# Optimization experiments

Hardware: AMD Instinct MI355X
Metric: run time of the kernel (lower is better)

## Reference

```python
import jax, jax.numpy as jnp
import numpy as np

N, E, F, H, L, G, EMB, C = 50000, 600000, 128, 128, 4, 64, 64, 10
BN_EPS = 1e-5


def setup_inputs() -> dict:
    key = jax.random.key(0)
    k = lambda i: jax.random.fold_in(key, i)
    s = 0.05  # weight scale
    return {
        "x": jax.random.normal(k(0), (N, F), jnp.float32),
        "edge_index": jax.random.randint(k(1), (2, E), 0, N, jnp.int64),
        "batch": jnp.sort(jax.random.randint(k(2), (N,), 0, G, jnp.int64)),
        "emb": jax.random.normal(k(3), (G, EMB), jnp.float32),
        "eps": jnp.zeros((L,), jnp.float32),
        "W1": jax.random.normal(k(4), (L, F, H), jnp.float32) * s,
        "b1": jnp.zeros((L, H), jnp.float32),
        "W2": jax.random.normal(k(5), (L, H, H), jnp.float32) * s,
        "b2": jnp.zeros((L, H), jnp.float32),
        "gamma": jnp.ones((L, H), jnp.float32),
        "beta": jnp.zeros((L, H), jnp.float32),
        "lin1_w": jax.random.normal(k(6), (L * H + EMB, 2 * H), jnp.float32) * s,
        "lin1_b": jnp.zeros((2 * H,), jnp.float32),
        "lin2_w": jax.random.normal(k(7), (2 * H, H), jnp.float32) * s,
        "lin2_b": jnp.zeros((H,), jnp.float32),
        "lin4_w": jax.random.normal(k(8), (H, C), jnp.float32) * s,
        "lin4_b": jnp.zeros((C,), jnp.float32),
    }


def _gin_mlp(h, W1, b1, W2, b2, gamma, beta):
    # Linear -> ReLU -> Linear -> ReLU -> BatchNorm1d (batch stats)
    h = jax.nn.relu(h @ W1 + b1)
    h = jax.nn.relu(h @ W2 + b2)
    mean = jnp.mean(h, axis=0)
    var = jnp.var(h, axis=0)
    return (h - mean) * jax.lax.rsqrt(var + BN_EPS) * gamma + beta


def reference(x, edge_index, batch, emb, eps, W1, b1, W2, b2, gamma, beta,
              lin1_w, lin1_b, lin2_w, lin2_b, lin4_w, lin4_b):
    src, dst = edge_index[0], edge_index[1]
    xs = []
    for l in range(L):
        # GIN: MLP((1+eps)*x_i + sum_{j->i} x_j)  via gather + scatter-add
        agg = jax.ops.segment_sum(x[src], dst, num_segments=N)  # [N,H]
        x = _gin_mlp((1.0 + eps[l]) * x + agg,
                     W1[l], b1[l], W2[l], b2[l], gamma[l], beta[l])
        xs.append(x)
    h = jnp.concatenate(xs, axis=1)  # [N, L*H]
    # global mean pool per graph
    sums = jax.ops.segment_sum(h, batch, num_segments=G)  # [G, L*H]
    cnt = jax.ops.segment_sum(jnp.ones((N,), h.dtype), batch, num_segments=G)
    pooled = sums / jnp.maximum(cnt, 1.0)[:, None]
    z = jnp.concatenate([pooled, emb.reshape(G, -1)], axis=1)
    z = jax.nn.relu(z @ lin1_w + lin1_b)  # .relu() twice is idempotent
    # dropout p=0.5 skipped (eval mode); lin3 unused in original forward
    z = jax.nn.relu(z @ lin2_w + lin2_b)
    z = z @ lin4_w + lin4_b
    return jax.nn.log_softmax(z, axis=1)
```

## Files before the change

### kernel.cpp

```cpp
#include <hip/hip_runtime.h>
#include <cstdint>
#include <cstddef>

#define N_NODES 50000
#define N_EDGES 600000
#define NLAYER  4
#define NGRAPH  64
#define SCAN_NB 196
#define NBLK_MLP ((N_NODES + 127) / 128)

typedef unsigned int   u32;
typedef unsigned short u16;
typedef unsigned char  u8;
typedef float f32x4  __attribute__((ext_vector_type(4)));
typedef short bf16x8 __attribute__((ext_vector_type(8)));

__device__ __forceinline__ u16 f2bf(float f) {
    u32 x = __float_as_uint(f);
    u32 r = x + 0x7fffu + ((x >> 16) & 1u);
    return (u16)(r >> 16);
}
__device__ __forceinline__ u32 pack2(float a, float b) {
    return (u32)f2bf(a) | ((u32)f2bf(b) << 16);
}

__device__ __forceinline__ float fp8b0(u32 u) { return __builtin_amdgcn_cvt_f32_fp8(u, 0); }
__device__ __forceinline__ float fp8b1(u32 u) { return __builtin_amdgcn_cvt_f32_fp8(u, 1); }
__device__ __forceinline__ u32 pk_fp8(float a, float b) {
    return (u32)__builtin_amdgcn_cvt_pk_fp8_f32(a, b, 0, false);
}

__global__ __launch_bounds__(256) void cvt_x(const float4* __restrict__ x,
                                             u32* __restrict__ xf8) {
    int i = blockIdx.x * 256 + threadIdx.x;
    if (i < N_NODES * 32) {
        float4 v = x[i];
        u32 r = pk_fp8(v.x, v.y);
        r = (u32)__builtin_amdgcn_cvt_pk_fp8_f32(v.z, v.w, (int)r, true);
        xf8[i] = r;
    }
}

__global__ __launch_bounds__(128) void cvt_w(const float* __restrict__ W1,
                                             const float* __restrict__ W2,
                                             short* __restrict__ W1t,
                                             short* __restrict__ W2t) {
    int l = blockIdx.y, n = blockIdx.x, k = threadIdx.x;
    const float* W = blockIdx.z ? W2 : W1;
    short* Wt      = blockIdx.z ? W2t : W1t;
    Wt[((size_t)l * 128 + n) * 128 + k] = (short)f2bf(W[((size_t)l * 128 + k) * 128 + n]);
}

__global__ void count_deg(const int* __restrict__ dst, int* __restrict__ deg) {
    int e = blockIdx.x * 256 + threadIdx.x;
    if (e < N_EDGES) atomicAdd(&deg[dst[e]], 1);
}

__global__ __launch_bounds__(256) void scan_l1(const int* __restrict__ deg,
                                               int* __restrict__ bscan,
                                               int* __restrict__ bsum) {
    __shared__ int sd[256];
    int tid = threadIdx.x;
    int i = blockIdx.x * 256 + tid;
    int v = (i < N_NODES) ? deg[i] : 0;
    sd[tid] = v; __syncthreads();
#pragma unroll
    for (int off = 1; off < 256; off <<= 1) {
        int t = (tid >= off) ? sd[tid - off] : 0;
        __syncthreads();
        sd[tid] += t; __syncthreads();
    }
    if (i < N_NODES) bscan[i] = sd[tid];
    if (tid == 255) bsum[blockIdx.x] = sd[255];
}

__global__ __launch_bounds__(256) void scan_l3(const int* __restrict__ bscan,
                                               const int* __restrict__ bsum,
                                               int* __restrict__ rowp) {
    __shared__ int sd[256];
    __shared__ int sboff;
    int tid = threadIdx.x;
    int v = (tid < SCAN_NB) ? bsum[tid] : 0;
    sd[tid] = v; __syncthreads();
#pragma unroll
    for (int off = 1; off < 256; off <<= 1) {
        int t = (tid >= off) ? sd[tid - off] : 0;
        __syncthreads();
        sd[tid] += t; __syncthreads();
    }
    if (tid == (int)blockIdx.x) sboff = sd[tid] - v;
    __syncthreads();
    int i = blockIdx.x * 256 + tid;
    if (i == 0) rowp[0] = 0;
    if (i < N_NODES) rowp[i + 1] = bscan[i] + sboff;
}

__global__ void fill_csr(const int* __restrict__ src, const int* __restrict__ dst,
                         const int* __restrict__ rowp, int* __restrict__ cursor,
                         int* __restrict__ col) {
    int e = blockIdx.x * 256 + threadIdx.x;
    if (e < N_EDGES) {
        int d = dst[e];
        int pos = atomicAdd(&cursor[d], 1);
        col[rowp[d] + pos] = src[e];
    }
}

__global__ __launch_bounds__(256) void agg_kernel(
    const u16* __restrict__ xin,
    const float* __restrict__ coef,
    const int* __restrict__ rowp, const int* __restrict__ col,
    const float* __restrict__ eps_all, int layer,
    u32* __restrict__ agg) {
    int node = blockIdx.x * 4 + (threadIdx.x >> 6);
    int lane = threadIdx.x & 63;
    if (node >= N_NODES) return;
    float a0 = 1.f, a1 = 1.f, d0 = 0.f, d1 = 0.f;
    if (coef) {
        a0 = coef[2 * lane];       a1 = coef[2 * lane + 1];
        d0 = coef[128 + 2 * lane]; d1 = coef[128 + 2 * lane + 1];
    }
    float ep = 1.0f + eps_all[layer];
    u32 v = xin[(size_t)node * 64 + lane];
    int k0 = rowp[node], k1 = rowp[node + 1];
    float s0 = 0.f, s1 = 0.f;
    int k = k0;
    int cc[8];
    if (k < k1) {
#pragma unroll
        for (int t = 0; t < 8; t++) cc[t] = col[min(k + t, k1 - 1)];
    }
    while (k < k1) {
        int idx[8];
#pragma unroll
        for (int t = 0; t < 8; t++) idx[t] = cc[t];
        int kn = k + 8;
        if (kn < k1) {
#pragma unroll
            for (int t = 0; t < 8; t++) cc[t] = col[min(kn + t, k1 - 1)];
        }
#pragma unroll
        for (int t = 0; t < 8; t++) {
            u32 u = xin[(size_t)idx[t] * 64 + lane];
            float w = (k + t < k1) ? 1.f : 0.f;
            s0 += w * fp8b0(u); s1 += w * fp8b1(u);
        }
        k = kn;
    }
    float deg = (float)(k1 - k0);
    float r0 = ep * (a0 * fp8b0(v) + d0) + a0 * s0 + deg * d0;
    float r1 = ep * (a1 * fp8b1(v) + d1) + a1 * s1 + deg * d1;
    agg[(size_t)node * 64 + lane] = pack2(r0, r1);
}

#define H1_STRIDE 136
__global__ __launch_bounds__(256) void mlp_fused(
    const short* __restrict__ A,
    const short* __restrict__ W1t, const float* __restrict__ b1,
    const short* __restrict__ W2t, const float* __restrict__ b2,
    u8* __restrict__ H2, const int* __restrict__ batch,
    float* __restrict__ sums, float* __restrict__ gsum, int M) {
    __shared__ alignas(16) short h1s[128 * H1_STRIDE];
    __shared__ int sh_ga, sh_gb, sh_split;
    int tid  = threadIdx.x;
    int wave = tid >> 6, lane = tid & 63;
    int ln15 = lane & 15, quad = lane >> 4;
    int m0blk = blockIdx.x * 128;
    int m0 = m0blk + wave * 32;
    const bf16x8 zz = {0, 0, 0, 0, 0, 0, 0, 0};

    if (tid == 0) {
        int rlo = m0blk, rhi = min(m0blk + 127, M - 1);
        int ga = batch[rlo], gb = batch[rhi];
        int split = m0blk + 128;
        if (ga != gb) {
            int lo = rlo, hi = rhi;
            while (lo + 1 < hi) { int mid = (lo + hi) >> 1; if (batch[mid] == ga) lo = mid; else hi = mid; }
            split = hi;
        }
        sh_ga = ga; sh_gb = gb; sh_split = split;
    }

    bf16x8 a[2][4];
#pragma unroll
    for (int rt = 0; rt < 2; rt++) {
        int row = m0 + rt * 16 + ln15;
        const short* rp = A + (size_t)row * 128 + quad * 8;
        bool ok = row < M;
#pragma unroll
        for (int s = 0; s < 4; s++)
            a[rt][s] = ok ? *(const bf16x8*)(rp + s * 32) : zz;
    }
#pragma unroll
    for (int ct = 0; ct < 8; ct++) {
        const short* wp = W1t + (size_t)(ct * 16 + ln15) * 128 + quad * 8;
        bf16x8 b[4];
#pragma unroll
        for (int s = 0; s < 4; s++) b[s] = *(const bf16x8*)(wp + s * 32);
        float bias = b1[ct * 16 + ln15];
#pragma unroll
        for (int rt = 0; rt < 2; rt++) {
            f32x4 acc = {0.f, 0.f, 0.f, 0.f};
#pragma unroll
            for (int s = 0; s < 4; s++)
                acc = __builtin_amdgcn_mfma_f32_16x16x32_bf16(a[rt][s], b[s], acc, 0, 0, 0);
#pragma unroll
            for (int i = 0; i < 4; i++) {
                float v = fmaxf(acc[i] + bias, 0.f);
                int lr = wave * 32 + rt * 16 + quad * 4 + i;
                h1s[lr * H1_STRIDE + ct * 16 + ln15] = (short)f2bf(v);
            }
        }
    }
    __syncthreads();
    bf16x8 c[2][4];
#pragma unroll
    for (int rt = 0; rt < 2; rt++) {
        const short* rp = h1s + (size_t)(wave * 32 + rt * 16 + ln15) * H1_STRIDE + quad * 8;
#pragma unroll
        for (int s = 0; s < 4; s++) c[rt][s] = *(const bf16x8*)(rp + s * 32);
    }
    int gsplit = sh_split;
    float sAcc[8], qAcc[8], pAcc[8];
#pragma unroll
    for (int ct = 0; ct < 8; ct++) { sAcc[ct] = 0.f; qAcc[ct] = 0.f; pAcc[ct] = 0.f; }
#pragma unroll
    for (int ct = 0; ct < 8; ct++) {
        const short* wp = W2t + (size_t)(ct * 16 + ln15) * 128 + quad * 8;
        bf16x8 b[4];
#pragma unroll
        for (int s = 0; s < 4; s++) b[s] = *(const bf16x8*)(wp + s * 32);
        float bias = b2[ct * 16 + ln15];
#pragma unroll
        for (int rt = 0; rt < 2; rt++) {
            f32x4 acc = {0.f, 0.f, 0.f, 0.f};
#pragma unroll
            for (int s = 0; s < 4; s++)
                acc = __builtin_amdgcn_mfma_f32_16x16x32_bf16(c[rt][s], b[s], acc, 0, 0, 0);
            int colx = ct * 16 + ln15;
#pragma unroll
            for (int i = 0; i < 4; i++) {
                int row = m0 + rt * 16 + quad * 4 + i;
                float v = fmaxf(acc[i] + bias, 0.f);
                if (row < M) H2[(size_t)row * 128 + colx] = (u8)(pk_fp8(v, v) & 0xffu);
                float vm = (row < M) ? v : 0.f;
                sAcc[ct] += vm; qAcc[ct] += vm * vm;
                if (row < gsplit) pAcc[ct] += vm;
            }
        }
    }
    __syncthreads();
    float* scr = (float*)h1s;
    int slice = wave * 4 + quad;
#pragma unroll
    for (int ct = 0; ct < 8; ct++) {
        int colx = ct * 16 + ln15;
        scr[(0 * 16 + slice) * 128 + colx] = sAcc[ct];
        scr[(1 * 16 + slice) * 128 + colx] = qAcc[ct];
        scr[(2 * 16 + slice) * 128 + colx] = pAcc[ct];
    }
    __syncthreads();
    if (tid < 128) {
        float ss = 0.f, qq = 0.f, pa = 0.f;
#pragma unroll
        for (int sl = 0; sl < 16; sl++) {
            ss += scr[(0 * 16 + sl) * 128 + tid];
            qq += scr[(1 * 16 + sl) * 128 + tid];
            pa += scr[(2 * 16 + sl) * 128 + tid];
        }
        atomicAdd(&sums[tid], ss);
        atomicAdd(&sums[128 + tid], qq);
        int ga = sh_ga, gb = sh_gb;
        atomicAdd(&gsum[ga * 128 + tid], pa);
        if (gb != ga) atomicAdd(&gsum[gb * 128 + tid], ss - pa);
    }
}

__global__ __launch_bounds__(128) void coef_fin(
    const float* __restrict__ sums,
    const float* __restrict__ gamma, const float* __restrict__ beta,
    int layer, float* __restrict__ coef) {
    int t = threadIdx.x;
    float s1 = sums[t];
    float s2 = sums[128 + t];
    float mean = s1 * (1.0f / N_NODES);
    float var  = s2 * (1.0f / N_NODES) - mean * mean;
    float a = rsqrtf(var + 1e-5f) * gamma[layer * 128 + t];
    coef[t]       = a;
    coef[128 + t] = beta[layer * 128 + t] - mean * a;
}

__global__ __launch_bounds__(256) void head_kernel(
    const float* __restrict__ gsum, const float* __restrict__ coefL,
    const int* __restrict__ batch, const float* __restrict__ emb,
    const float* __restrict__ l1w, const float* __restrict__ l1b,
    const float* __restrict__ l2w, const float* __restrict__ l2b,
    const float* __restrict__ l4w, const float* __restrict__ l4b,
    float* __restrict__ out) {
    __shared__ float z[576];
    __shared__ float z1[256];
    __shared__ float z2h[2][128];
    __shared__ float z2[128];
    __shared__ float zr[128][10];
    __shared__ float inv_cnt;
    int g = blockIdx.x;
    int tid = threadIdx.x;
    if (tid == 0) {
        int lo = 0, hi = N_NODES;
        while (lo < hi) { int m = (lo + hi) >> 1; if (batch[m] < g) lo = m + 1; else hi = m; }
        int s = lo;
        lo = 0; hi = N_NODES;
        while (lo < hi) { int m = (lo + hi) >> 1; if (batch[m] < g + 1) lo = m + 1; else hi = m; }
        inv_cnt = 1.0f / fmaxf((float)(lo - s), 1.0f);
    }
    __syncthreads();
    for (int j = tid; j < 512; j += 256) {
        int l = j >> 7, c = j & 127;
        float a = coefL[l * 256 + c], d = coefL[l * 256 + 128 + c];
        z[j] = a * gsum[(size_t)l * NGRAPH * 128 + g * 128 + c] * inv_cnt + d;
    }
    if (tid < 64) z[512 + tid] = emb[g * 64 + tid];
    __syncthreads();
    {
        float acc = l1b[tid];
        for (int j0 = 0; j0 < 576; j0 += 16) {
            float lw[16];
#pragma unroll
            for (int t = 0; t < 16; t++) lw[t] = l1w[(j0 + t) * 256 + tid];
#pragma unroll
            for (int t = 0; t < 16; t++) acc += z[j0 + t] * lw[t];
        }
        z1[tid] = fmaxf(acc, 0.f);
    }
    __syncthreads();
    {
        int c2 = tid & 127, half = tid >> 7;
        float acc = 0.f;
        int jb = half * 128;
        for (int j0 = 0; j0 < 128; j0 += 8) {
            float lw[8];
#pragma unroll
            for (int t = 0; t < 8; t++) lw[t] = l2w[(jb + j0 + t) * 128 + c2];
#pragma unroll
            for (int t = 0; t < 8; t++) acc += z1[jb + j0 + t] * lw[t];
        }
        z2h[half][c2] = acc;
    }
    __syncthreads();
    if (tid < 128) z2[tid] = fmaxf(z2h[0][tid] + z2h[1][tid] + l2b[tid], 0.f);
    __syncthreads();
    if (tid < 128) {
        float zv = z2[tid];
        const float* wr = l4w + tid * 10;
#pragma unroll
        for (int c = 0; c < 10; c++) zr[tid][c] = zv * wr[c];
    }
    __syncthreads();
    for (int s = 64; s >= 1; s >>= 1) {
        if (tid < s) {
#pragma unroll
            for (int c = 0; c < 10; c++) zr[tid][c] += zr[tid + s][c];
        }
        __syncthreads();
    }
    if (tid == 0) {
        float z3s[10];
#pragma unroll
        for (int c = 0; c < 10; c++) z3s[c] = zr[0][c] + l4b[c];
        float m = z3s[0];
        for (int i = 1; i < 10; i++) m = fmaxf(m, z3s[i]);
        float se = 0.f;
        for (int i = 0; i < 10; i++) se += expf(z3s[i] - m);
        float lse = m + logf(se);
        for (int i = 0; i < 10; i++) out[g * 10 + i] = z3s[i] - lse;
    }
}

extern "C" void kernel_launch(void* const* d_in, const int* in_sizes, int n_in,
                              void* d_out, int out_size, void* d_ws, size_t ws_size,
                              hipStream_t stream) {
    (void)in_sizes; (void)n_in; (void)out_size; (void)ws_size;
    const float* x0   = (const float*)d_in[0];
    const int* ei     = (const int*)d_in[1];
    const int* src    = ei;
    const int* dst    = ei + N_EDGES;
    const int* batch  = (const int*)d_in[2];
    const float* emb  = (const float*)d_in[3];
    const float* eps  = (const float*)d_in[4];
    const float* W1   = (const float*)d_in[5];
    const float* b1   = (const float*)d_in[6];
    const float* W2   = (const float*)d_in[7];
    const float* b2   = (const float*)d_in[8];
    const float* gamma= (const float*)d_in[9];
    const float* beta = (const float*)d_in[10];
    const float* l1w  = (const float*)d_in[11];
    const float* l1b  = (const float*)d_in[12];
    const float* l2w  = (const float*)d_in[13];
    const float* l2b  = (const float*)d_in[14];
    const float* l4w  = (const float*)d_in[15];
    const float* l4b  = (const float*)d_in[16];

    char* ws = (char*)d_ws;
    size_t off = 0;
    auto alloc = [&](size_t bytes) -> char* {
        char* p = ws + off; off += (bytes + 255) & ~(size_t)255; return p;
    };
    int* deg    = (int*)alloc(N_NODES * 4);
    int* cursor = (int*)alloc(N_NODES * 4);
    float* sumsL = (float*)alloc(NLAYER * 256 * 4);
    float* gsumL = (float*)alloc((size_t)NLAYER * NGRAPH * 128 * 4);
    size_t zero_len = (char*)gsumL - (char*)deg + (size_t)NLAYER * NGRAPH * 128 * 4;
    int* rowp   = (int*)alloc((N_NODES + 1) * 4);
    int* bscan  = (int*)alloc(N_NODES * 4);
    int* bsum   = (int*)alloc(SCAN_NB * 4);
    int* col    = (int*)alloc(N_EDGES * 4);
    u8* xf8     = (u8*)alloc((size_t)N_NODES * 128);
    u8* h2a     = (u8*)alloc((size_t)N_NODES * 128);
    u8* h2b     = (u8*)alloc((size_t)N_NODES * 128);
    u32* agg    = (u32*)alloc((size_t)N_NODES * 64 * 4);
    short* W1t  = (short*)alloc((size_t)NLAYER * 128 * 128 * 2);
    short* W2t  = (short*)alloc((size_t)NLAYER * 128 * 128 * 2);
    float* coefL = (float*)alloc(NLAYER * 256 * 4);

    hipMemsetAsync(deg, 0, zero_len, stream);

    cvt_x<<<(N_NODES * 32 + 255) / 256, 256, 0, stream>>>((const float4*)x0, (u32*)xf8);
    {
        dim3 gw(128, NLAYER, 2);
        cvt_w<<<gw, 128, 0, stream>>>(W1, W2, W1t, W2t);
    }
    count_deg<<<(N_EDGES + 255) / 256, 256, 0, stream>>>(dst, deg);
    scan_l1<<<SCAN_NB, 256, 0, stream>>>(deg, bscan, bsum);
    scan_l3<<<SCAN_NB, 256, 0, stream>>>(bscan, bsum, rowp);
    fill_csr<<<(N_EDGES + 255) / 256, 256, 0, stream>>>(src, dst, rowp, cursor, col);

    const u8* xin = xf8;
    for (int l = 0; l < NLAYER; ++l) {
        u8* h2 = (l & 1) ? h2b : h2a;
        const float* coef_prev = (l == 0) ? nullptr : (coefL + (l - 1) * 256);
        agg_kernel<<<(N_NODES + 3) / 4, 256, 0, stream>>>(
            (const u16*)xin, coef_prev, rowp, col, eps, l, agg);
        mlp_fused<<<NBLK_MLP, 256, 0, stream>>>(
            (const short*)agg, W1t + (size_t)l * 16384, b1 + l * 128,
            W2t + (size_t)l * 16384, b2 + l * 128, h2, batch,
            sumsL + l * 256, gsumL + (size_t)l * NGRAPH * 128, N_NODES);
        coef_fin<<<1, 128, 0, stream>>>(sumsL + l * 256, gamma, beta, l,
                                        coefL + l * 256);
        xin = h2;
    }
    head_kernel<<<NGRAPH, 256, 0, stream>>>(gsumL, coefL, batch, emb,
                                            l1w, l1b, l2w, l2b, l4w, l4b,
                                            (float*)d_out);
}
```

Baseline: 409.4 us.

## Fuse neighbor aggregation into the MLP kernel and merge setup kernels

Neighbor aggregation is folded into the per-layer MLP kernel, so aggregated rows go straight into LDS instead of a global bf16 buffer. Each block now handles 64 rows, and each wave aggregates 16 nodes one after another with col prefetch. BatchNorm coefficient finalization moves into the consumer kernels, removing the coef_fin launches. The three setup kernels are merged into one launch. The aim is to cut global round trips and launch count, at the cost of serial per-wave aggregation and half-sized MFMA tiles per wave.

```diff
diff --git a/kernel.cpp b/kernel.cpp
--- a/kernel.cpp
+++ b/kernel.cpp
@@ -7,7 +7,11 @@
 #define NLAYER  4
 #define NGRAPH  64
 #define SCAN_NB 196
-#define NBLK_MLP ((N_NODES + 127) / 128)
+#define LROWS   64
+#define NBLK_L  ((N_NODES + LROWS - 1) / LROWS)
+#define CVTX_NB ((N_NODES * 32 + 255) / 256)
+#define CVTW_NB ((NLAYER * 128 * 128 * 2) / 256)
+#define DEG_NB  ((N_EDGES + 255) / 256)
 
 typedef unsigned int   u32;
 typedef unsigned short u16;
@@ -30,30 +34,31 @@
     return (u32)__builtin_amdgcn_cvt_pk_fp8_f32(a, b, 0, false);
 }
 
-__global__ __launch_bounds__(256) void cvt_x(const float4* __restrict__ x,
-                                             u32* __restrict__ xf8) {
-    int i = blockIdx.x * 256 + threadIdx.x;
-    if (i < N_NODES * 32) {
-        float4 v = x[i];
-        u32 r = pk_fp8(v.x, v.y);
-        r = (u32)__builtin_amdgcn_cvt_pk_fp8_f32(v.z, v.w, (int)r, true);
-        xf8[i] = r;
-    }
-}
-
-__global__ __launch_bounds__(128) void cvt_w(const float* __restrict__ W1,
-                                             const float* __restrict__ W2,
-                                             short* __restrict__ W1t,
-                                             short* __restrict__ W2t) {
-    int l = blockIdx.y, n = blockIdx.x, k = threadIdx.x;
-    const float* W = blockIdx.z ? W2 : W1;
-    short* Wt      = blockIdx.z ? W2t : W1t;
-    Wt[((size_t)l * 128 + n) * 128 + k] = (short)f2bf(W[((size_t)l * 128 + k) * 128 + n]);
-}
-
-__global__ void count_deg(const int* __restrict__ dst, int* __restrict__ deg) {
-    int e = blockIdx.x * 256 + threadIdx.x;
-    if (e < N_EDGES) atomicAdd(&deg[dst[e]], 1);
+__global__ __launch_bounds__(256) void setup_all(
+    const float4* __restrict__ x, u32* __restrict__ xf8,
+    const float* __restrict__ W1, const float* __restrict__ W2,
+    short* __restrict__ W1t, short* __restrict__ W2t,
+    const int* __restrict__ dst, int* __restrict__ deg) {
+    int b = blockIdx.x, tid = threadIdx.x;
+    if (b < CVTX_NB) {
+        int i = b * 256 + tid;
+        if (i < N_NODES * 32) {
+            float4 v = x[i];
+            u32 r = pk_fp8(v.x, v.y);
+            r = (u32)__builtin_amdgcn_cvt_pk_fp8_f32(v.z, v.w, (int)r, true);
+            xf8[i] = r;
+        }
+    } else if (b < CVTX_NB + CVTW_NB) {
+        int i = (b - CVTX_NB) * 256 + tid;
+        int z = i >> 16, r = i & 65535;
+        int l = r >> 14, n = (r >> 7) & 127, k = r & 127;
+        const float* W = z ? W2 : W1;
+        short* Wt      = z ? W2t : W1t;
+        Wt[((size_t)l * 128 + n) * 128 + k] = (short)f2bf(W[((size_t)l * 128 + k) * 128 + n]);
+    } else {
+        int e = (b - CVTX_NB - CVTW_NB) * 256 + tid;
+        if (e < N_EDGES) atomicAdd(&deg[dst[e]], 1);
+    }
 }
 
 __global__ __launch_bounds__(256) void scan_l1(const int* __restrict__ deg,
@@ -106,73 +111,39 @@
     }
 }
 
-__global__ __launch_bounds__(256) void agg_kernel(
+__global__ __launch_bounds__(256) void layer_fused(
     const u16* __restrict__ xin,
-    const float* __restrict__ coef,
+    const float* __restrict__ sums_prev,
+    const float* __restrict__ gamma, const float* __restrict__ beta,
+    int layer, const float* __restrict__ eps_all,
     const int* __restrict__ rowp, const int* __restrict__ col,
-    const float* __restrict__ eps_all, int layer,
-    u32* __restrict__ agg) {
-    int node = blockIdx.x * 4 + (threadIdx.x >> 6);
-    int lane = threadIdx.x & 63;
-    if (node >= N_NODES) return;
-    float a0 = 1.f, a1 = 1.f, d0 = 0.f, d1 = 0.f;
-    if (coef) {
-        a0 = coef[2 * lane];       a1 = coef[2 * lane + 1];
-        d0 = coef[128 + 2 * lane]; d1 = coef[128 + 2 * lane + 1];
-    }
-    float ep = 1.0f + eps_all[layer];
-    u32 v = xin[(size_t)node * 64 + lane];
-    int k0 = rowp[node], k1 = rowp[node + 1];
-    float s0 = 0.f, s1 = 0.f;
-    int k = k0;
-    int cc[8];
-    if (k < k1) {
-#pragma unroll
-        for (int t = 0; t < 8; t++) cc[t] = col[min(k + t, k1 - 1)];
-    }
-    while (k < k1) {
-        int idx[8];
-#pragma unroll
-        for (int t = 0; t < 8; t++) idx[t] = cc[t];
-        int kn = k + 8;
-        if (kn < k1) {
-#pragma unroll
-            for (int t = 0; t < 8; t++) cc[t] = col[min(kn + t, k1 - 1)];
-        }
-#pragma unroll
-        for (int t = 0; t < 8; t++) {
-            u32 u = xin[(size_t)idx[t] * 64 + lane];
-            float w = (k + t < k1) ? 1.f : 0.f;
-            s0 += w * fp8b0(u); s1 += w * fp8b1(u);
-        }
-        k = kn;
-    }
-    float deg = (float)(k1 - k0);
-    float r0 = ep * (a0 * fp8b0(v) + d0) + a0 * s0 + deg * d0;
-    float r1 = ep * (a1 * fp8b1(v) + d1) + a1 * s1 + deg * d1;
-    agg[(size_t)node * 64 + lane] = pack2(r0, r1);
-}
-
-#define H1_STRIDE 136
-__global__ __launch_bounds__(256) void mlp_fused(
-    const short* __restrict__ A,
     const short* __restrict__ W1t, const float* __restrict__ b1,
     const short* __restrict__ W2t, const float* __restrict__ b2,
     u8* __restrict__ H2, const int* __restrict__ batch,
     float* __restrict__ sums, float* __restrict__ gsum, int M) {
-    __shared__ alignas(16) short h1s[128 * H1_STRIDE];
+    __shared__ alignas(16) u32 buf[LROWS * 68];
+    __shared__ float cA[128], cD[128];
     __shared__ int sh_ga, sh_gb, sh_split;
     int tid  = threadIdx.x;
     int wave = tid >> 6, lane = tid & 63;
     int ln15 = lane & 15, quad = lane >> 4;
-    int m0blk = blockIdx.x * 128;
-    int m0 = m0blk + wave * 32;
-    const bf16x8 zz = {0, 0, 0, 0, 0, 0, 0, 0};
-
+    int m0blk = blockIdx.x * LROWS;
+
+    if (tid < 128) {
+        float a = 1.f, d = 0.f;
+        if (sums_prev) {
+            float s1 = sums_prev[tid], s2 = sums_prev[128 + tid];
+            float mean = s1 * (1.0f / N_NODES);
+            float var  = s2 * (1.0f / N_NODES) - mean * mean;
+            a = rsqrtf(var + 1e-5f) * gamma[(layer - 1) * 128 + tid];
+            d = beta[(layer - 1) * 128 + tid] - mean * a;
+        }
+        cA[tid] = a; cD[tid] = d;
+    }
     if (tid == 0) {
-        int rlo = m0blk, rhi = min(m0blk + 127, M - 1);
+        int rlo = m0blk, rhi = min(m0blk + LROWS - 1, M - 1);
         int ga = batch[rlo], gb = batch[rhi];
-        int split = m0blk + 128;
+        int split = m0blk + LROWS;
         if (ga != gb) {
             int lo = rlo, hi = rhi;
             while (lo + 1 < hi) { int mid = (lo + hi) >> 1; if (batch[mid] == ga) lo = mid; else hi = mid; }
@@ -180,17 +151,70 @@
         }
         sh_ga = ga; sh_gb = gb; sh_split = split;
     }
-
-    bf16x8 a[2][4];
-#pragma unroll
-    for (int rt = 0; rt < 2; rt++) {
-        int row = m0 + rt * 16 + ln15;
-        const short* rp = A + (size_t)row * 128 + quad * 8;
-        bool ok = row < M;
-#pragma unroll
-        for (int s = 0; s < 4; s++)
-            a[rt][s] = ok ? *(const bf16x8*)(rp + s * 32) : zz;
-    }
+    __syncthreads();
+
+    {
+        float a0 = cA[2 * lane], a1 = cA[2 * lane + 1];
+        float d0 = cD[2 * lane], d1 = cD[2 * lane + 1];
+        float ep = 1.0f + eps_all[layer];
+        int nodebase = m0blk + wave * 16;
+        int rp = rowp[min(nodebase + lane, N_NODES)];
+        int k0 = __shfl(rp, 0), k1 = __shfl(rp, 1);
+        int cc[8], nn[8];
+        if (k0 < k1) {
+#pragma unroll
+            for (int t = 0; t < 8; t++) cc[t] = col[min(k0 + t, k1 - 1)];
+        }
+        for (int i = 0; i < 16; i++) {
+            int node = nodebase + i;
+            int row  = wave * 16 + i;
+            int nk1  = __shfl(rp, min(i + 2, 16));
+            if (i < 15 && k1 < nk1) {
+#pragma unroll
+                for (int t = 0; t < 8; t++) nn[t] = col[min(k1 + t, nk1 - 1)];
+            }
+            if (node < M) {
+                u32 v = xin[(size_t)node * 64 + lane];
+                float s0 = 0.f, s1 = 0.f;
+                int k = k0;
+                while (k < k1) {
+                    int idx[8];
+#pragma unroll
+                    for (int t = 0; t < 8; t++) idx[t] = cc[t];
+                    int kn = k + 8;
+                    if (kn < k1) {
+#pragma unroll
+                        for (int t = 0; t < 8; t++) cc[t] = col[min(kn + t, k1 - 1)];
+                    }
+#pragma unroll
+                    for (int t = 0; t < 8; t++) {
+                        u32 u = xin[(size_t)idx[t] * 64 + lane];
+                        float w = (k + t < k1) ? 1.f : 0.f;
+                        s0 += w * fp8b0(u); s1 += w * fp8b1(u);
+                    }
+                    k = kn;
+                }
+                float dg = (float)(k1 - k0);
+                float r0 = ep * (a0 * fp8b0(v) + d0) + a0 * s0 + dg * d0;
+                float r1 = ep * (a1 * fp8b1(v) + d1) + a1 * s1 + dg * d1;
+                buf[row * 68 + lane] = pack2(r0, r1);
+            } else {
+                buf[row * 68 + lane] = 0u;
+            }
+            k0 = k1; k1 = nk1;
+#pragma unroll
+            for (int t = 0; t < 8; t++) cc[t] = nn[t];
+        }
+    }
+    __syncthreads();
+
+    bf16x8 a[4];
+#pragma unroll
+    for (int s = 0; s < 4; s++)
+        a[s] = *(const bf16x8*)&buf[(wave * 16 + ln15) * 68 + quad * 4 + s * 16];
+    __syncthreads();
+
+    short* h1s = (short*)buf;
 #pragma unroll
     for (int ct = 0; ct < 8; ct++) {
         const short* wp = W1t + (size_t)(ct * 16 + ln15) * 128 + quad * 8;
@@ -198,28 +222,25 @@
 #pragma unroll
         for (int s = 0; s < 4; s++) b[s] = *(const bf16x8*)(wp + s * 32);
         float bias = b1[ct * 16 + ln15];
-#pragma unroll
-        for (int rt = 0; rt < 2; rt++) {
-            f32x4 acc = {0.f, 0.f, 0.f, 0.f};
-#pragma unroll
-            for (int s = 0; s < 4; s++)
-                acc = __builtin_amdgcn_mfma_f32_16x16x32_bf16(a[rt][s], b[s], acc, 0, 0, 0);
-#pragma unroll
-            for (int i = 0; i < 4; i++) {
-                float v = fmaxf(acc[i] + bias, 0.f);
-                int lr = wave * 32 + rt * 16 + quad * 4 + i;
-                h1s[lr * H1_STRIDE + ct * 16 + ln15] = (short)f2bf(v);
-            }
-        }
-    }
-    __syncthreads();
-    bf16x8 c[2][4];
-#pragma unroll
-    for (int rt = 0; rt < 2; rt++) {
-        const short* rp = h1s + (size_t)(wave * 32 + rt * 16 + ln15) * H1_STRIDE + quad * 8;
-#pragma unroll
-        for (int s = 0; s < 4; s++) c[rt][s] = *(const bf16x8*)(rp + s * 32);
-    }
+        f32x4 acc = {0.f, 0.f, 0.f, 0.f};
+#pragma unroll
+        for (int s = 0; s < 4; s++)
+            acc = __builtin_amdgcn_mfma_f32_16x16x32_bf16(a[s], b[s], acc, 0, 0, 0);
+#pragma unroll
+        for (int i = 0; i < 4; i++) {
+            float v = fmaxf(acc[i] + bias, 0.f);
+            int lr = wave * 16 + quad * 4 + i;
+            h1s[lr * 136 + ct * 16 + ln15] = (short)f2bf(v);
+        }
+    }
+    __syncthreads();
+
+    bf16x8 c[4];
+#pragma unroll
+    for (int s = 0; s < 4; s++)
+        c[s] = *(const bf16x8*)&h1s[(wave * 16 + ln15) * 136 + quad * 8 + s * 32];
+    __syncthreads();
+
     int gsplit = sh_split;
     float sAcc[8], qAcc[8], pAcc[8];
 #pragma unroll
@@ -231,42 +252,45 @@
 #pragma unroll
         for (int s = 0; s < 4; s++) b[s] = *(const bf16x8*)(wp + s * 32);
         float bias = b2[ct * 16 + ln15];
-#pragma unroll
-        for (int rt = 0; rt < 2; rt++) {
-            f32x4 acc = {0.f, 0.f, 0.f, 0.f};
-#pragma unroll
-            for (int s = 0; s < 4; s++)
-                acc = __builtin_amdgcn_mfma_f32_16x16x32_bf16(c[rt][s], b[s], acc, 0, 0, 0);
+        f32x4 acc = {0.f, 0.f, 0.f, 0.f};
+#pragma unroll
+        for (int s = 0; s < 4; s++)
+            acc = __builtin_amdgcn_mfma_f32_16x16x32_bf16(c[s], b[s], acc, 0, 0, 0);
+        int colx = ct * 16 + ln15;
+#pragma unroll
+        for (int i = 0; i < 4; i++) {
+            int row = m0blk + wave * 16 + quad * 4 + i;
+            float v = fmaxf(acc[i] + bias, 0.f);
+            if (row < M) H2[(size_t)row * 128 + colx] = (u8)(pk_fp8(v, v) & 0xffu);
+            float vm = (row < M) ? v : 0.f;
+            sAcc[ct] += vm; qAcc[ct] += vm * vm;
+            if (row < gsplit) pAcc[ct] += vm;
+        }
+    }
+#pragma unroll
+    for (int ct = 0; ct < 8; ct++) {
+        sAcc[ct] += __shfl_xor(sAcc[ct], 16); sAcc[ct] += __shfl_xor(sAcc[ct], 32);
+        qAcc[ct] += __shfl_xor(qAcc[ct], 16); qAcc[ct] += __shfl_xor(qAcc[ct], 32);
+        pAcc[ct] += __shfl_xor(pAcc[ct], 16); pAcc[ct] += __shfl_xor(pAcc[ct], 32);
+    }
+    float* scr = (float*)buf;
+    if (quad == 0) {
+#pragma unroll
+        for (int ct = 0; ct < 8; ct++) {
             int colx = ct * 16 + ln15;
-#pragma unroll
-            for (int i = 0; i < 4; i++) {
-                int row = m0 + rt * 16 + quad * 4 + i;
-                float v = fmaxf(acc[i] + bias, 0.f);
-                if (row < M) H2[(size_t)row * 128 + colx] = (u8)(pk_fp8(v, v) & 0xffu);
-                float vm = (row < M) ? v : 0.f;
-                sAcc[ct] += vm; qAcc[ct] += vm * vm;
-                if (row < gsplit) pAcc[ct] += vm;
-            }
-        }
-    }
-    __syncthreads();
-    float* scr = (float*)h1s;
-    int slice = wave * 4 + quad;
-#pragma unroll
-    for (int ct = 0; ct < 8; ct++) {
-        int colx = ct * 16 + ln15;
-        scr[(0 * 16 + slice) * 128 + colx] = sAcc[ct];
-        scr[(1 * 16 + slice) * 128 + colx] = qAcc[ct];
-        scr[(2 * 16 + slice) * 128 + colx] = pAcc[ct];
+            scr[(0 * 4 + wave) * 128 + colx] = sAcc[ct];
+            scr[(1 * 4 + wave) * 128 + colx] = qAcc[ct];
+            scr[(2 * 4 + wave) * 128 + colx] = pAcc[ct];
+        }
     }
     __syncthreads();
     if (tid < 128) {
         float ss = 0.f, qq = 0.f, pa = 0.f;
 #pragma unroll
-        for (int sl = 0; sl < 16; sl++) {
-            ss += scr[(0 * 16 + sl) * 128 + tid];
-            qq += scr[(1 * 16 + sl) * 128 + tid];
-            pa += scr[(2 * 16 + sl) * 128 + tid];
+        for (int w = 0; w < 4; w++) {
+            ss += scr[(0 * 4 + w) * 128 + tid];
+            qq += scr[(1 * 4 + w) * 128 + tid];
+            pa += scr[(2 * 4 + w) * 128 + tid];
         }
         atomicAdd(&sums[tid], ss);
         atomicAdd(&sums[128 + tid], qq);
@@ -276,22 +300,9 @@
     }
 }
 
-__global__ __launch_bounds__(128) void coef_fin(
-    const float* __restrict__ sums,
+__global__ __launch_bounds__(256) void head_kernel(
+    const float* __restrict__ gsum, const float* __restrict__ sumsL,
     const float* __restrict__ gamma, const float* __restrict__ beta,
-    int layer, float* __restrict__ coef) {
-    int t = threadIdx.x;
-    float s1 = sums[t];
-    float s2 = sums[128 + t];
-    float mean = s1 * (1.0f / N_NODES);
-    float var  = s2 * (1.0f / N_NODES) - mean * mean;
-    float a = rsqrtf(var + 1e-5f) * gamma[layer * 128 + t];
-    coef[t]       = a;
-    coef[128 + t] = beta[layer * 128 + t] - mean * a;
-}
-
-__global__ __launch_bounds__(256) void head_kernel(
-    const float* __restrict__ gsum, const float* __restrict__ coefL,
     const int* __restrict__ batch, const float* __restrict__ emb,
     const float* __restrict__ l1w, const float* __restrict__ l1b,
     const float* __restrict__ l2w, const float* __restrict__ l2b,
@@ -316,7 +327,11 @@
     __syncthreads();
     for (int j = tid; j < 512; j += 256) {
         int l = j >> 7, c = j & 127;
-        float a = coefL[l * 256 + c], d = coefL[l * 256 + 128 + c];
+        float s1 = sumsL[l * 256 + c], s2 = sumsL[l * 256 + 128 + c];
+        float mean = s1 * (1.0f / N_NODES);
+        float var  = s2 * (1.0f / N_NODES) - mean * mean;
+        float a = rsqrtf(var + 1e-5f) * gamma[l * 128 + c];
+        float d = beta[l * 128 + c] - mean * a;
         z[j] = a * gsum[(size_t)l * NGRAPH * 128 + g * 128 + c] * inv_cnt + d;
     }
     if (tid < 64) z[512 + tid] = emb[g * 64 + tid];
@@ -417,19 +432,13 @@
     u8* xf8     = (u8*)alloc((size_t)N_NODES * 128);
     u8* h2a     = (u8*)alloc((size_t)N_NODES * 128);
     u8* h2b     = (u8*)alloc((size_t)N_NODES * 128);
-    u32* agg    = (u32*)alloc((size_t)N_NODES * 64 * 4);
     short* W1t  = (short*)alloc((size_t)NLAYER * 128 * 128 * 2);
     short* W2t  = (short*)alloc((size_t)NLAYER * 128 * 128 * 2);
-    float* coefL = (float*)alloc(NLAYER * 256 * 4);
 
     hipMemsetAsync(deg, 0, zero_len, stream);
 
-    cvt_x<<<(N_NODES * 32 + 255) / 256, 256, 0, stream>>>((const float4*)x0, (u32*)xf8);
-    {
-        dim3 gw(128, NLAYER, 2);
-        cvt_w<<<gw, 128, 0, stream>>>(W1, W2, W1t, W2t);
-    }
-    count_deg<<<(N_EDGES + 255) / 256, 256, 0, stream>>>(dst, deg);
+    setup_all<<<CVTX_NB + CVTW_NB + DEG_NB, 256, 0, stream>>>(
+        (const float4*)x0, (u32*)xf8, W1, W2, W1t, W2t, dst, deg);
     scan_l1<<<SCAN_NB, 256, 0, stream>>>(deg, bscan, bsum);
     scan_l3<<<SCAN_NB, 256, 0, stream>>>(bscan, bsum, rowp);
     fill_csr<<<(N_EDGES + 255) / 256, 256, 0, stream>>>(src, dst, rowp, cursor, col);
@@ -437,18 +446,16 @@
     const u8* xin = xf8;
     for (int l = 0; l < NLAYER; ++l) {
         u8* h2 = (l & 1) ? h2b : h2a;
-        const float* coef_prev = (l == 0) ? nullptr : (coefL + (l - 1) * 256);
-        agg_kernel<<<(N_NODES + 3) / 4, 256, 0, stream>>>(
-            (const u16*)xin, coef_prev, rowp, col, eps, l, agg);
-        mlp_fused<<<NBLK_MLP, 256, 0, stream>>>(
-            (const short*)agg, W1t + (size_t)l * 16384, b1 + l * 128,
-            W2t + (size_t)l * 16384, b2 + l * 128, h2, batch,
-            sumsL + l * 256, gsumL + (size_t)l * NGRAPH * 128, N_NODES);
-        coef_fin<<<1, 128, 0, stream>>>(sumsL + l * 256, gamma, beta, l,
-                                        coefL + l * 256);
+        const float* sums_prev = (l == 0) ? nullptr : (sumsL + (l - 1) * 256);
+        layer_fused<<<NBLK_L, 256, 0, stream>>>(
+            (const u16*)xin, sums_prev, gamma, beta, l, eps,
+            rowp, col,
+            W1t + (size_t)l * 16384, b1 + l * 128,
+            W2t + (size_t)l * 16384, b2 + l * 128,
+            h2, batch, sumsL + l * 256, gsumL + (size_t)l * NGRAPH * 128, N_NODES);
         xin = h2;
     }
-    head_kernel<<<NGRAPH, 256, 0, stream>>>(gsumL, coefL, batch, emb,
+    head_kernel<<<NGRAPH, 256, 0, stream>>>(gsumL, sumsL, gamma, beta, batch, emb,
                                             l1w, l1b, l2w, l2b, l4w, l4b,
                                             (float*)d_out);
 }
```

New measurement: 486.8 us. 1.19x slower.

## Balance aggregation by splitting a block's edge range evenly across waves

Applied to the files above, without the earlier changes.

Replaces the one-wave-per-node CSR gather with a block that owns 64 destination nodes and divides their combined edge range evenly among four waves. Each wave finds an edge's destination row by binary search over the block's row pointers in shared memory. It accumulates partial sums in registers and flushes them to a shared-memory accumulator with atomics whenever the row changes. A final pass applies the epsilon and BN-coefficient affine step and writes bf16 output. This is meant to remove load imbalance from varying node degrees, at the cost of shared-memory atomics, binary searches and an extra synchronisation.

```diff
diff --git a/kernel.cpp b/kernel.cpp
--- a/kernel.cpp
+++ b/kernel.cpp
@@ -8,6 +8,9 @@
 #define NGRAPH  64
 #define SCAN_NB 196
 #define NBLK_MLP ((N_NODES + 127) / 128)
+#define DBLK    64
+#define AGG_NB  ((N_NODES + DBLK - 1) / DBLK)
+#define ACC_STR 132
 
 typedef unsigned int   u32;
 typedef unsigned short u16;
@@ -106,51 +109,105 @@
     }
 }
 
-__global__ __launch_bounds__(256) void agg_kernel(
+__global__ __launch_bounds__(256) void agg_edges(
     const u16* __restrict__ xin,
     const float* __restrict__ coef,
     const int* __restrict__ rowp, const int* __restrict__ col,
     const float* __restrict__ eps_all, int layer,
     u32* __restrict__ agg) {
-    int node = blockIdx.x * 4 + (threadIdx.x >> 6);
-    int lane = threadIdx.x & 63;
-    if (node >= N_NODES) return;
-    float a0 = 1.f, a1 = 1.f, d0 = 0.f, d1 = 0.f;
-    if (coef) {
-        a0 = coef[2 * lane];       a1 = coef[2 * lane + 1];
-        d0 = coef[128 + 2 * lane]; d1 = coef[128 + 2 * lane + 1];
-    }
-    float ep = 1.0f + eps_all[layer];
-    u32 v = xin[(size_t)node * 64 + lane];
-    int k0 = rowp[node], k1 = rowp[node + 1];
+    __shared__ float acc[DBLK * ACC_STR];
+    __shared__ float cA[128], cD[128];
+    __shared__ int rps[DBLK + 1];
+    int tid = threadIdx.x, wave = tid >> 6, lane = tid & 63;
+    int m0 = blockIdx.x * DBLK;
+
+    if (tid <= DBLK) rps[tid] = rowp[min(m0 + tid, N_NODES)];
+    if (tid < 128) {
+        cA[tid] = coef ? coef[tid] : 1.f;
+        cD[tid] = coef ? coef[128 + tid] : 0.f;
+    }
+    for (int i = tid; i < DBLK * ACC_STR; i += 256) acc[i] = 0.f;
+    __syncthreads();
+
+    int E0 = rps[0], E1 = rps[DBLK];
+    int nE = E1 - E0;
+    int per = (nE + 3) >> 2;
+    int e  = E0 + wave * per;
+    int e1 = min(e + per, E1);
+
+    auto findrow = [&](int eq) {
+        int lo = 0, hi = DBLK;
+#pragma unroll
+        for (int it = 0; it < 6; ++it) {
+            int mid = (lo + hi) >> 1;
+            if (rps[mid] <= eq) lo = mid; else hi = mid;
+        }
+        return lo;
+    };
+
     float s0 = 0.f, s1 = 0.f;
-    int k = k0;
-    int cc[8];
-    if (k < k1) {
-#pragma unroll
-        for (int t = 0; t < 8; t++) cc[t] = col[min(k + t, k1 - 1)];
-    }
-    while (k < k1) {
-        int idx[8];
-#pragma unroll
-        for (int t = 0; t < 8; t++) idx[t] = cc[t];
-        int kn = k + 8;
-        if (kn < k1) {
-#pragma unroll
-            for (int t = 0; t < 8; t++) cc[t] = col[min(kn + t, k1 - 1)];
+    int cur = -1;
+    int cc[8], dd8[8];
+    if (e < e1) {
+#pragma unroll
+        for (int t = 0; t < 8; t++) cc[t] = col[min(e + t, e1 - 1)];
+        int da = findrow(min(e + (lane & 7), e1 - 1));
+#pragma unroll
+        for (int t = 0; t < 8; t++) dd8[t] = __shfl(da, t);
+        cur = dd8[0];
+    }
+    while (e < e1) {
+        int idx[8], dct[8];
+#pragma unroll
+        for (int t = 0; t < 8; t++) { idx[t] = cc[t]; dct[t] = dd8[t]; }
+        u32 uu[8];
+#pragma unroll
+        for (int t = 0; t < 8; t++) uu[t] = xin[(unsigned)idx[t] * 64u + lane];
+        int en = e + 8;
+        if (en < e1) {
+#pragma unroll
+            for (int t = 0; t < 8; t++) cc[t] = col[min(en + t, e1 - 1)];
+            int da = findrow(min(en + (lane & 7), e1 - 1));
+#pragma unroll
+            for (int t = 0; t < 8; t++) dd8[t] = __shfl(da, t);
         }
 #pragma unroll
         for (int t = 0; t < 8; t++) {
-            u32 u = xin[(size_t)idx[t] * 64 + lane];
-            float w = (k + t < k1) ? 1.f : 0.f;
-            s0 += w * fp8b0(u); s1 += w * fp8b1(u);
-        }
-        k = kn;
-    }
-    float deg = (float)(k1 - k0);
-    float r0 = ep * (a0 * fp8b0(v) + d0) + a0 * s0 + deg * d0;
-    float r1 = ep * (a1 * fp8b1(v) + d1) + a1 * s1 + deg * d1;
-    agg[(size_t)node * 64 + lane] = pack2(r0, r1);
+            bool ok = (e + t < e1);
+            if (ok && dct[t] != cur) {
+                atomicAdd(&acc[cur * ACC_STR + 2 * lane], s0);
+                atomicAdd(&acc[cur * ACC_STR + 2 * lane + 1], s1);
+                s0 = 0.f; s1 = 0.f; cur = dct[t];
+            }
+            float w = ok ? 1.f : 0.f;
+            s0 += w * fp8b0(uu[t]); s1 += w * fp8b1(uu[t]);
+        }
+        e = en;
+    }
+    if (cur >= 0) {
+        atomicAdd(&acc[cur * ACC_STR + 2 * lane], s0);
+        atomicAdd(&acc[cur * ACC_STR + 2 * lane + 1], s1);
+    }
+    __syncthreads();
+
+    {
+        float ep = 1.0f + eps_all[layer];
+        float A0 = cA[2 * lane], A1 = cA[2 * lane + 1];
+        float D0 = cD[2 * lane], D1 = cD[2 * lane + 1];
+        int rbase = wave * 16;
+#pragma unroll 4
+        for (int i = 0; i < 16; i++) {
+            int row = rbase + i;
+            int node = m0 + row;
+            if (node >= N_NODES) break;
+            float dg = (float)(rps[row + 1] - rps[row]);
+            u32 u = xin[(unsigned)node * 64u + lane];
+            float2 S = *(const float2*)&acc[row * ACC_STR + 2 * lane];
+            float r0 = ep * (A0 * fp8b0(u) + D0) + A0 * S.x + dg * D0;
+            float r1 = ep * (A1 * fp8b1(u) + D1) + A1 * S.y + dg * D1;
+            agg[(unsigned)node * 64u + lane] = pack2(r0, r1);
+        }
+    }
 }
 
 #define H1_STRIDE 136
@@ -438,7 +495,7 @@
     for (int l = 0; l < NLAYER; ++l) {
         u8* h2 = (l & 1) ? h2b : h2a;
         const float* coef_prev = (l == 0) ? nullptr : (coefL + (l - 1) * 256);
-        agg_kernel<<<(N_NODES + 3) / 4, 256, 0, stream>>>(
+        agg_edges<<<AGG_NB, 256, 0, stream>>>(
             (const u16*)xin, coef_prev, rowp, col, eps, l, agg);
         mlp_fused<<<NBLK_MLP, 256, 0, stream>>>(
             (const short*)agg, W1t + (size_t)l * 16384, b1 + l * 128,
```

New measurement: 595.1 us. 45.4% more time.
